# Optimization experiments

Measured on AMD Instinct MI355X. Metric: run time of the kernel, lower is better.

The kernel has to match this reference:

```python
import jax, jax.numpy as jnp
from jax import lax
import numpy as np

# Module config (from init_kwargs)
NUM_SEG_ROW = 8
NUM_SEG_COL = 8
H = 224
W = 224
K = NUM_SEG_ROW * NUM_SEG_COL  # 64 labels
B = 4


def setup_inputs() -> dict:
    key = jax.random.key(0)
    grad_map = jax.random.normal(key, (B, 1, H, W), dtype=jnp.float32)
    return {"grad_map": grad_map, "band_width": 5, "num_iterations": 5}


def _dp_paths(neg_g):
    """Dynamic-programming min-cost path. neg_g: (L, P, M) per-step costs.
    Returns positions (L, P): index in [0, M) chosen at each step."""
    L, P, M = neg_g.shape
    m = jnp.arange(M)
    # clamp(m + {-1,0,1}, 0, M-1); torch's inf padding is never hit after clamping
    nbr = jnp.clip(m[:, None] + jnp.array([-1, 0, 1])[None, :], 0, M - 1)  # (M,3)

    def step(prev_cost, g_row):
        pc = prev_cost[:, nbr]                      # (P, M, 3)
        amin = pc.argmin(axis=2)                    # (P, M)
        min_prev = jnp.take_along_axis(pc, amin[..., None], axis=2)[..., 0]
        path_row = nbr[m[None, :], amin]            # (P, M) predecessor position
        new_cost = min_prev + g_row
        return new_cost, (new_cost, path_row)

    _, (costs, paths) = lax.scan(step, neg_g[0], neg_g[1:])  # paths: (L-1, P, M)
    idx_last = costs[-1].argmin(axis=1)             # (P,)

    def back(idx, path_row):
        new_idx = path_row[jnp.arange(path_row.shape[0]), idx]
        return new_idx, idx

    first_idx, pos_tail = lax.scan(back, idx_last, paths, reverse=True)
    positions = jnp.concatenate([first_idx[None], pos_tail], axis=0)  # (L, P)
    return positions


def _boundary_masks(grad2d, x_inits, y_inits, band_width):
    """grad2d: (H, W). Returns (vmask, hmask) boolean (H, W)."""
    offs = jnp.arange(-band_width, band_width + 1)
    P = x_inits.shape[0]
    # vertical paths (one x per row)
    x_idx = jnp.clip(x_inits[:, None] + offs[None, :], 0, W - 1)   # (P, M)
    pos_v = _dp_paths(-grad2d[:, x_idx])                            # (H, P)
    coords_v = x_idx[jnp.arange(P)[None, :], pos_v]                 # (H, P) x-coords
    vmask = jnp.zeros((H, W), bool).at[jnp.arange(H)[:, None], coords_v].set(True)
    # horizontal paths (one y per column)
    y_idx = jnp.clip(y_inits[:, None] + offs[None, :], 0, H - 1)    # (P, M)
    pos_h = _dp_paths(-grad2d.T[:, y_idx])                          # (W, P)
    coords_h = y_idx[jnp.arange(P)[None, :], pos_h]                 # (W, P) y-coords
    hmask = jnp.zeros((H, W), bool).at[coords_h, jnp.arange(W)[:, None]].set(True)
    return vmask, hmask


def _one_hot_nchw(labels):
    return jax.nn.one_hot(labels, K, dtype=jnp.float32).transpose(0, 3, 1, 2)


def _box_vote(oh, ksize):
    # grouped (depthwise) conv with all-ones kernel == neighborhood vote count
    kern = jnp.ones((K, 1, ksize, ksize), oh.dtype)
    pad = ksize // 2
    return lax.conv_general_dilated(
        oh, kern, window_strides=(1, 1), padding=[(pad, pad), (pad, pad)],
        dimension_numbers=("NCHW", "OIHW", "NCHW"), feature_group_count=K)


def reference(grad_map, band_width, num_iterations):
    x_inits = jnp.clip(jnp.array([i * (W // NUM_SEG_COL) for i in range(1, NUM_SEG_COL)]), 0, W - 1)
    y_inits = jnp.clip(jnp.array([i * (H // NUM_SEG_ROW) for i in range(1, NUM_SEG_ROW)]), 0, H - 1)
    vmask, hmask = jax.vmap(lambda g: _boundary_masks(g, x_inits, y_inits, band_width))(grad_map[:, 0])
    v_labels = jnp.cumsum(vmask.astype(jnp.int32), axis=2)
    h_labels = jnp.cumsum(hmask.astype(jnp.int32), axis=1)
    seg = v_labels + NUM_SEG_COL * h_labels                         # (B, H, W), values in [0, K)
    # multi-scale connectivity voting
    oh = _one_hot_nchw(seg)
    labels = seg
    for _ in range(num_iterations):
        vote_sum = _box_vote(oh, 3) + _box_vote(oh, 5) + _box_vote(oh, 7)
        labels = vote_sum.argmax(axis=1)
        oh = _one_hot_nchw(labels)
    return labels
```

## Files before the change

### kernel.cpp

```cpp
#include <hip/hip_runtime.h>
#include <stdint.h>

#define HH 224
#define WW 224
#define BB 4
#define PP 7
#define SEG 28
#define BW 5
#define MM 11

#define POS_INF_I 0x7F800000

typedef const __attribute__((address_space(1))) unsigned int* gas_ptr;
typedef __attribute__((address_space(3))) unsigned int* las_ptr;

__device__ inline unsigned long long mcompose(unsigned long long F, unsigned long long G) {
    unsigned long long H = 0ull;
#pragma unroll
    for (int i = 0; i < 11; ++i) {
        unsigned g = (unsigned)(G >> (4 * i)) & 15u;
        H |= ((F >> (4 * g)) & 15ull) << (4 * i);
    }
    return H;
}

__global__ __launch_bounds__(64) void dp_kernel(const float* __restrict__ grad,
                                                int* __restrict__ coords_v,
                                                int* __restrict__ coords_h) {
    __shared__ __align__(16) float gseg[225 * 16];

    const int tid = threadIdx.x;
    const int l   = tid & 15;
    const int sid = blockIdx.x;
    const int p   = sid % PP;
    const int dir = (sid / PP) & 1;
    const int b   = sid / (2 * PP);
    const int base = SEG * (p + 1);
    const float* gb = grad + b * (HH * WW);

    {
        const int r  = tid >> 4;
        const int m  = tid & 15;
        const int sS = (dir == 0) ? WW : 1;
        const int sM = (dir == 0) ? 1  : WW;
        const float* src = gb + r * sS + (base - BW + m) * sM;
        const long stepBytes = (long)(4 * sS) * 4;
#pragma unroll 8
        for (int c = 0; c < 56; ++c) {
            __builtin_amdgcn_global_load_lds((gas_ptr)(const void*)src,
                                             (las_ptr)(void*)(&gseg[c * 64]), 4, 0, 0);
            src = (const float*)((const char*)src + stepBytes);
        }
    }
    __syncthreads();

    const float lane_add = (l < MM) ? 0.0f : __int_as_float(POS_INF_I);
    const float* gp = &gseg[l];

    unsigned wreg[16] = {};

#define DP_STEP(gval, ownb, jj_c)                                                       \
    {                                                                                   \
        float v1 = cost;                                                                \
        float v0 = __int_as_float(__builtin_amdgcn_update_dpp(                          \
            POS_INF_I, __float_as_int(cost), 0x111, 0xf, 0xf, false));                  \
        float v2 = __int_as_float(__builtin_amdgcn_update_dpp(                          \
            POS_INF_I, __float_as_int(cost), 0x101, 0xf, 0xf, false));                  \
        bool a01 = (v0 <= v1), a02 = (v0 <= v2), a12 = (v1 <= v2);                      \
        bool aa  = a01 && a02;                                                          \
        unsigned long long A   = __ballot(aa);                                          \
        unsigned long long C12 = __ballot(a12);                                         \
        unsigned long long B0 = ~A & C12;                                               \
        unsigned long long B1 = ~A & ~C12;                                              \
        float mv = aa ? v0 : (a12 ? v1 : v2);                                           \
        cost = mv - (gval) + lane_add;                                                  \
        unsigned wv = (unsigned)(B0 & 0x7FFull) | ((unsigned)(B1 & 0x7FFull) << 11);    \
        wreg[(jj_c)] = (ownb) ? wv : wreg[(jj_c)];                                      \
    }

    float cost = -gp[0] + lane_add;
    float buf[16], c0[16];
#pragma unroll
    for (int k = 0; k < 16; ++k) buf[k] = gp[(1 + k) * 16];
    for (int t = 0; t < 13; ++t) {
        const bool own = (tid == t);
#pragma unroll
        for (int k = 0; k < 16; ++k) c0[k] = buf[k];
#pragma unroll
        for (int k = 0; k < 16; ++k) buf[k] = gp[(16 * (t + 1) + 1 + k) * 16];
#pragma unroll
        for (int k = 0; k < 16; ++k) DP_STEP(c0[k], own, k)
    }
    {
        const bool own = (tid == 13);
#pragma unroll
        for (int k = 0; k < 15; ++k) DP_STEP(buf[k], own, k)
    }
#undef DP_STEP

    float bc = cost;
    int   bi = l;
#pragma unroll
    for (int mask = 1; mask < 16; mask <<= 1) {
        float oc = __shfl_xor(bc, mask, 16);
        int   oi = __shfl_xor(bi, mask, 16);
        if (oc < bc || (oc == bc && oi < bi)) { bc = oc; bi = oi; }
    }
    const int idx_last = bi;

    const int mcnt = (l < 13) ? 16 : ((l == 13) ? 15 : 0);
    const unsigned long long IDMAP = 0xA9876543210ull;
    unsigned long long L = IDMAP;
#pragma unroll
    for (int jj = 15; jj >= 0; --jj) {
        if (jj < mcnt) {
            unsigned ww = wreg[jj];
            unsigned long long M = 0ull;
#pragma unroll
            for (int i = 0; i < MM; ++i) {
                unsigned sel = ((ww >> i) & 1u) + 2u * ((ww >> (11 + i)) & 1u);
                M |= ((unsigned long long)(i + (int)sel - 1)) << (4 * i);
            }
            L = mcompose(M, L);
        }
    }
    unsigned long long I = L;
#pragma unroll
    for (int d = 1; d < 16; d <<= 1) {
        unsigned long long O = __shfl_down(I, d, 16);
        if (l + d < 16) I = mcompose(I, O);
    }
    unsigned long long R = __shfl_down(I, 1, 16);
    if (l == 15) R = IDMAP;

    int* cout = (dir == 0) ? coords_v : coords_h;
    if (tid == 15) cout[(b * HH + 223) * PP + p] = base + idx_last - BW;
    if (tid < 16) {
        unsigned v = (unsigned)(R >> (4 * idx_last)) & 15u;
#pragma unroll
        for (int jj = 15; jj >= 0; --jj) {
            if (jj < mcnt) {
                unsigned ww = wreg[jj];
                unsigned sel = ((ww >> v) & 1u) + 2u * ((ww >> (11 + v)) & 1u);
                v = v + sel - 1u;
                cout[(b * HH + (16 * l + jj)) * PP + p] = base + (int)v - BW;
            }
        }
    }
}

#define RW 38
#define RH 14
#define RSTR 40

__global__ __launch_bounds__(256) void labvote_kernel(const int* __restrict__ cv,
                                                      const int* __restrict__ ch,
                                                      unsigned char* __restrict__ out8) {
    __shared__ unsigned char lab[RH * RSTR];
    __shared__ unsigned bins[16 * 256];
    const int tx = threadIdx.x, ty = threadIdx.y;
    const int t  = ty * 32 + tx;
    const int b  = blockIdx.z;
    const int GX0 = blockIdx.x * 32, GY0 = blockIdx.y * 8;

    for (int idx = t; idx < RW * RH; idx += 256) {
        int j = idx / RW, i = idx - j * RW;
        int gx = GX0 - 3 + i, gy = GY0 - 3 + j;
        if ((unsigned)gx < WW && (unsigned)gy < HH) {
            const int* cvp = cv + (b * HH + gy) * PP;
            const int* chp = ch + (b * WW + gx) * PP;
            int v = 0, h = 0;
#pragma unroll
            for (int q = 0; q < PP; ++q) { v += (cvp[q] <= gx); h += (chp[q] <= gy); }
            lab[j * RSTR + i] = (unsigned char)(v + 8 * h);
        }
    }
    __syncthreads();

    const int gx = GX0 + tx, gy = GY0 + ty;
#pragma unroll
    for (int c = 0; c < 16; ++c) bins[c * 256 + t] = 0u;
#pragma unroll
    for (int dy = -3; dy <= 3; ++dy) {
        if ((unsigned)(gy + dy) >= HH) continue;
#pragma unroll
        for (int dx = -3; dx <= 3; ++dx) {
            if ((unsigned)(gx + dx) >= WW) continue;
            int lb = lab[(ty + 3 + dy) * RSTR + (tx + 3 + dx)];
            int ay = dy < 0 ? -dy : dy, ax = dx < 0 ? -dx : dx;
            int d = ay > ax ? ay : ax;
            unsigned wgt = (d <= 1) ? 3u : (unsigned)(4 - d);
            atomicAdd(&bins[(lb >> 2) * 256 + t], wgt << ((lb & 3) * 8));
        }
    }
    int best_s = 0, best_k = 0;
#pragma unroll
    for (int c = 0; c < 16; ++c) {
        unsigned wd = bins[c * 256 + t];
        if (wd) {
#pragma unroll
            for (int q = 0; q < 4; ++q) {
                int s = (int)((wd >> (q * 8)) & 255u);
                if (s > best_s) { best_s = s; best_k = c * 4 + q; }
            }
        }
    }
    out8[(b * HH + gy) * WW + gx] = (unsigned char)best_k;
}

__global__ __launch_bounds__(256) void vote_kernel(const unsigned char* __restrict__ in,
                                                   unsigned char* __restrict__ out8,
                                                   int* __restrict__ out32) {
    __shared__ unsigned bins[17 * 256];
    const int tx = threadIdx.x, ty = threadIdx.y;
    const int t  = ty * 32 + tx;
    const int x  = blockIdx.x * 32 + tx;
    const int y  = blockIdx.y * 8 + ty;
    const int b  = blockIdx.z;
    const unsigned char* img = in + b * (HH * WW);

#pragma unroll
    for (int c = 0; c < 17; ++c) bins[c * 256 + t] = 0u;

#pragma unroll
    for (int dy = -3; dy <= 3; ++dy) {
        int yy = y + dy;
        bool oky = (unsigned)yy < (unsigned)HH;
        int yc = min(max(yy, 0), HH - 1);
#pragma unroll
        for (int dx = -3; dx <= 3; ++dx) {
            int xx = x + dx;
            bool ok = oky && ((unsigned)xx < (unsigned)WW);
            int xc = min(max(xx, 0), WW - 1);
            int lab = img[yc * WW + xc];
            lab = ok ? lab : 64;
            const int ady = dy < 0 ? -dy : dy;
            const int adx = dx < 0 ? -dx : dx;
            const int d = ady > adx ? ady : adx;
            const unsigned wgt = (d <= 1) ? 3u : (unsigned)(4 - d);
            atomicAdd(&bins[(lab >> 2) * 256 + t], wgt << ((lab & 3) * 8));
        }
    }

    int best_s = -1, best_k = 0;
#pragma unroll
    for (int c = 0; c < 16; ++c) {
        unsigned wd = bins[c * 256 + t];
#pragma unroll
        for (int q = 0; q < 4; ++q) {
            int s = (int)((wd >> (q * 8)) & 255u);
            if (s > best_s) { best_s = s; best_k = c * 4 + q; }
        }
    }

    int o = b * (HH * WW) + y * WW + x;
    if (out8)  out8[o]  = (unsigned char)best_k;
    if (out32) out32[o] = best_k;
}

extern "C" void kernel_launch(void* const* d_in, const int* in_sizes, int n_in,
                              void* d_out, int out_size, void* d_ws, size_t ws_size,
                              hipStream_t stream) {
    const float* grad = (const float*)d_in[0];
    int* out = (int*)d_out;
    char* ws = (char*)d_ws;

    int* cv = (int*)(ws);
    int* ch = (int*)(ws + 25088);
    unsigned char* laW = (unsigned char*)(ws + 50176);
    unsigned char* laD = (unsigned char*)d_out;

    dp_kernel<<<56, 64, 0, stream>>>(grad, cv, ch);

    dim3 grid(WW / 32, HH / 8, BB), blk(32, 8, 1);
    labvote_kernel<<<grid, blk, 0, stream>>>(cv, ch, laD);
    vote_kernel<<<grid, blk, 0, stream>>>(laD, laW, nullptr);
    vote_kernel<<<grid, blk, 0, stream>>>(laW, laD, nullptr);
    vote_kernel<<<grid, blk, 0, stream>>>(laD, laW, nullptr);
    vote_kernel<<<grid, blk, 0, stream>>>(laW, nullptr, out);
}
```

Measured before the change: 123.4 us.

## Pack 7x7 label windows into registers and skip voting on uniform windows

The vote kernel now loads each 7-pixel row of the neighborhood as packed bytes using aligned 32-bit loads, with a scalar fallback for blocks on the x edges. If all 49 labels equal the center label, it outputs that label directly and skips the shared-memory histogram, the atomics and the argmax scan. Otherwise it runs the atomic voting as before, skipping out-of-range pixels instead of routing them to a 17th dummy bin. Since most pixels in piecewise-constant label maps sit in uniform regions, this removes most LDS atomic traffic, at the cost of extra branch divergence along label boundaries.

```diff
diff --git a/kernel.cpp b/kernel.cpp
--- a/kernel.cpp
+++ b/kernel.cpp
@@ -13,9 +13,10 @@
 
 typedef const __attribute__((address_space(1))) unsigned int* gas_ptr;
 typedef __attribute__((address_space(3))) unsigned int* las_ptr;
-
-__device__ inline unsigned long long mcompose(unsigned long long F, unsigned long long G) {
-    unsigned long long H = 0ull;
+typedef unsigned long long ull;
+
+__device__ inline ull mcompose(ull F, ull G) {
+    ull H = 0ull;
 #pragma unroll
     for (int i = 0; i < 11; ++i) {
         unsigned g = (unsigned)(G >> (4 * i)) & 15u;
@@ -109,28 +110,28 @@
     const int idx_last = bi;
 
     const int mcnt = (l < 13) ? 16 : ((l == 13) ? 15 : 0);
-    const unsigned long long IDMAP = 0xA9876543210ull;
-    unsigned long long L = IDMAP;
+    const ull IDMAP = 0xA9876543210ull;
+    ull L = IDMAP;
 #pragma unroll
     for (int jj = 15; jj >= 0; --jj) {
         if (jj < mcnt) {
             unsigned ww = wreg[jj];
-            unsigned long long M = 0ull;
+            ull M = 0ull;
 #pragma unroll
             for (int i = 0; i < MM; ++i) {
                 unsigned sel = ((ww >> i) & 1u) + 2u * ((ww >> (11 + i)) & 1u);
-                M |= ((unsigned long long)(i + (int)sel - 1)) << (4 * i);
+                M |= ((ull)(i + (int)sel - 1)) << (4 * i);
             }
             L = mcompose(M, L);
         }
     }
-    unsigned long long I = L;
+    ull I = L;
 #pragma unroll
     for (int d = 1; d < 16; d <<= 1) {
-        unsigned long long O = __shfl_down(I, d, 16);
+        ull O = __shfl_down(I, d, 16);
         if (l + d < 16) I = mcompose(I, O);
     }
-    unsigned long long R = __shfl_down(I, 1, 16);
+    ull R = __shfl_down(I, 1, 16);
     if (l == 15) R = IDMAP;
 
     int* cout = (dir == 0) ? coords_v : coords_h;
@@ -211,7 +212,7 @@
 __global__ __launch_bounds__(256) void vote_kernel(const unsigned char* __restrict__ in,
                                                    unsigned char* __restrict__ out8,
                                                    int* __restrict__ out32) {
-    __shared__ unsigned bins[17 * 256];
+    __shared__ unsigned bins[16 * 256];
     const int tx = threadIdx.x, ty = threadIdx.y;
     const int t  = ty * 32 + tx;
     const int x  = blockIdx.x * 32 + tx;
@@ -219,41 +220,79 @@
     const int b  = blockIdx.z;
     const unsigned char* img = in + b * (HH * WW);
 
-#pragma unroll
-    for (int c = 0; c < 17; ++c) bins[c * 256 + t] = 0u;
-
-#pragma unroll
-    for (int dy = -3; dy <= 3; ++dy) {
-        int yy = y + dy;
-        bool oky = (unsigned)yy < (unsigned)HH;
-        int yc = min(max(yy, 0), HH - 1);
-#pragma unroll
-        for (int dx = -3; dx <= 3; ++dx) {
-            int xx = x + dx;
-            bool ok = oky && ((unsigned)xx < (unsigned)WW);
-            int xc = min(max(xx, 0), WW - 1);
-            int lab = img[yc * WW + xc];
-            lab = ok ? lab : 64;
-            const int ady = dy < 0 ? -dy : dy;
-            const int adx = dx < 0 ? -dx : dx;
-            const int d = ady > adx ? ady : adx;
-            const unsigned wgt = (d <= 1) ? 3u : (unsigned)(4 - d);
-            atomicAdd(&bins[(lab >> 2) * 256 + t], wgt << ((lab & 3) * 8));
-        }
-    }
-
-    int best_s = -1, best_k = 0;
-#pragma unroll
-    for (int c = 0; c < 16; ++c) {
-        unsigned wd = bins[c * 256 + t];
-#pragma unroll
-        for (int q = 0; q < 4; ++q) {
-            int s = (int)((wd >> (q * 8)) & 255u);
-            if (s > best_s) { best_s = s; best_k = c * 4 + q; }
-        }
-    }
-
-    int o = b * (HH * WW) + y * WW + x;
+    ull rows[7];
+    const bool xedge = (blockIdx.x == 0) || (blockIdx.x == (WW / 32 - 1));
+    if (!xedge) {
+        const unsigned* img32 = (const unsigned*)img;
+        const int o0 = x - 3;
+#pragma unroll
+        for (int dy = -3; dy <= 3; ++dy) {
+            int yc = min(max(y + dy, 0), HH - 1);
+            int o  = yc * WW + o0;
+            int a  = o >> 2;
+            int sh = (o & 3) * 8;
+            unsigned d0 = img32[a], d1 = img32[a + 1], d2 = img32[a + 2];
+            ull lo = ((ull)d1 << 32) | d0;
+            ull row = lo >> sh;
+            if (sh) row |= (ull)d2 << (64 - sh);
+            rows[dy + 3] = row & 0x00FFFFFFFFFFFFFFull;
+        }
+    } else {
+#pragma unroll
+        for (int dy = -3; dy <= 3; ++dy) {
+            int yc = min(max(y + dy, 0), HH - 1);
+            ull row = 0ull;
+#pragma unroll
+            for (int dx = -3; dx <= 3; ++dx) {
+                int xc = min(max(x + dx, 0), WW - 1);
+                row |= (ull)img[yc * WW + xc] << (8 * (dx + 3));
+            }
+            rows[dy + 3] = row;
+        }
+    }
+
+    const unsigned labc = (unsigned)((rows[3] >> 24) & 255u);
+    const ull rep = (ull)labc * 0x0001010101010101ull;
+    bool uni = true;
+#pragma unroll
+    for (int k = 0; k < 7; ++k) uni = uni && (rows[k] == rep);
+
+    int best_k;
+    if (uni) {
+        best_k = (int)labc;
+    } else {
+#pragma unroll
+        for (int c = 0; c < 16; ++c) bins[c * 256 + t] = 0u;
+#pragma unroll
+        for (int dy = -3; dy <= 3; ++dy) {
+            if ((unsigned)(y + dy) >= (unsigned)HH) continue;
+            ull row = rows[dy + 3];
+            const int ay = dy < 0 ? -dy : dy;
+#pragma unroll
+            for (int dx = -3; dx <= 3; ++dx) {
+                if ((unsigned)(x + dx) >= (unsigned)WW) continue;
+                int lb = (int)((row >> (8 * (dx + 3))) & 255u);
+                const int ax = dx < 0 ? -dx : dx;
+                const int d = ay > ax ? ay : ax;
+                const unsigned wgt = (d <= 1) ? 3u : (unsigned)(4 - d);
+                atomicAdd(&bins[(lb >> 2) * 256 + t], wgt << ((lb & 3) * 8));
+            }
+        }
+        int best_s = 0; best_k = 0;
+#pragma unroll
+        for (int c = 0; c < 16; ++c) {
+            unsigned wd = bins[c * 256 + t];
+            if (wd) {
+#pragma unroll
+                for (int q = 0; q < 4; ++q) {
+                    int s = (int)((wd >> (q * 8)) & 255u);
+                    if (s > best_s) { best_s = s; best_k = c * 4 + q; }
+                }
+            }
+        }
+    }
+
+    int o = (b * HH + y) * WW + x;
     if (out8)  out8[o]  = (unsigned char)best_k;
     if (out32) out32[o] = best_k;
 }
```

Measured after the change: 119.3 us. 3.3% less time.
